# Kernel tuning notes

Measured on AMD Instinct MI355X. Metric: run time of the kernel, lower is better.

The kernel has to match this reference:

```python
import jax, jax.numpy as jnp
import numpy as np

L = 160        # voxel grid side
BATCH = 4
N_SAMPLE = 62500
N = 64


def _build_coords():
    rng = np.random.default_rng(0)
    coords = []
    for b in range(BATCH):
        c = np.unique(rng.integers(0, L, (N_SAMPLE, 3)), axis=0)  # sorted, unique
        bc = np.concatenate([np.full((len(c), 1), b, dtype=np.int64), c.astype(np.int64)], axis=1)
        coords.append(bc)
    return np.concatenate(coords, axis=0)  # [P,4] = (batch, x, y, z), globally key-sorted


def _neighbor_table(C):
    # integer key per coordinate; coords are unique+sorted so keys are strictly increasing
    keys = ((C[:, 0] * L + C[:, 1]) * L + C[:, 2]) * L + C[:, 3]
    P = C.shape[0]
    offs = np.array([[dx, dy, dz] for dx in (-1, 0, 1) for dy in (-1, 0, 1) for dz in (-1, 0, 1)], dtype=np.int64)
    nbr = np.full((P, 27), -1, dtype=np.int32)
    for k, o in enumerate(offs):
        nc = C[:, 1:] + o
        valid = np.all((nc >= 0) & (nc < L), axis=1)
        nk = ((C[:, 0] * L + nc[:, 0]) * L + nc[:, 1]) * L + nc[:, 2]
        pos = np.clip(np.searchsorted(keys, nk), 0, P - 1)
        found = valid & (keys[pos] == nk)
        nbr[:, k] = np.where(found, pos, -1).astype(np.int32)
    return nbr


def setup_inputs() -> dict:
    C = _build_coords()
    nbr = _neighbor_table(C)
    P = C.shape[0]
    key = jax.random.key(0)
    ks = jax.random.split(key, 10)
    s = 0.05  # small weight scale keeps activations well-conditioned
    return {
        "feats": jax.random.normal(ks[0], (P, N), jnp.float32),
        "cond": jax.random.normal(ks[1], (P, 2 * N), jnp.float32),
        "W1a": jax.random.normal(ks[2], (27, N, N), jnp.float32) * s,
        "b1a": jax.random.normal(ks[3], (N,), jnp.float32) * s,
        "W1b": jax.random.normal(ks[4], (27, N, N), jnp.float32) * s,
        "b1b": jax.random.normal(ks[5], (N,), jnp.float32) * s,
        "W2a": jax.random.normal(ks[6], (27, N, N), jnp.float32) * s,
        "b2a": jax.random.normal(ks[7], (N,), jnp.float32) * s,
        "W2b": jax.random.normal(ks[8], (27, N, N), jnp.float32) * s,
        "b2b": jax.random.normal(ks[9], (N,), jnp.float32) * s,
        "nbr": jnp.asarray(nbr),
    }


def _sparse_conv(x, nbr, W, b):
    # x: [P,N] features, nbr: [P,27] neighbor indices (-1 = missing)
    mask = (nbr >= 0)
    idx = jnp.maximum(nbr, 0)
    acc0 = jnp.zeros((x.shape[0], W.shape[2]), x.dtype)

    def body(acc, kin):
        wk, ik, mk = kin            # wk:[N,N], ik:[P], mk:[P]
        g = x[ik] * mk[:, None].astype(x.dtype)
        return acc + g @ wk, None

    out, _ = jax.lax.scan(body, acc0, (W, idx.T, mask.T))
    return out + b


def reference(feats, cond, W1a, b1a, W1b, b1b, W2a, b2a, W2b, b2b, nbr):
    x_res = feats
    # conv_1: conv -> relu -> conv
    h = _sparse_conv(feats, nbr, W1a, b1a)
    h = jax.nn.relu(h)
    h = _sparse_conv(h, nbr, W1b, b1b)
    # FiLM from condition (features_at_coordinates at identical coords -> direct lookup)
    beta, gamma = jnp.split(cond, 2, axis=1)
    h = h * beta + gamma
    # conv_2: conv -> relu -> conv -> relu
    h = _sparse_conv(h, nbr, W2a, b2a)
    h = jax.nn.relu(h)
    h = _sparse_conv(h, nbr, W2b, b2b)
    h = jax.nn.relu(h)
    # residual: x_res at same coordinates is an identity lookup
    return h + x_res
```

## Files before the change

### kernel.cpp

```cpp
#include <hip/hip_runtime.h>
#include <hip/hip_bf16.h>


#define N 64
#define TAPS 27
#define MT 256

typedef unsigned short u16;
typedef __attribute__((ext_vector_type(8))) short short8;
typedef __attribute__((ext_vector_type(16))) float floatx16;

__device__ __forceinline__ float bf2f(u16 v) {
    union { unsigned u; float f; } c;
    c.u = ((unsigned)v) << 16;
    return c.f;
}
__device__ __forceinline__ u16 f2bf(float f) {
    __hip_bfloat16 h = __float2bfloat16(f);
    u16 r;
    __builtin_memcpy(&r, &h, 2);
    return r;
}
__device__ __forceinline__ void split2(float x, u16& hi, u16& lo) {
    hi = f2bf(x);
    lo = f2bf(x - bf2f(hi));
}

__global__ void split_feats(const float* __restrict__ x, u16* __restrict__ hl, int n) {
    int i = blockIdx.x * 256 + threadIdx.x;
    if (i >= n) return;
    int p = i >> 6, c = i & 63;
    u16 h, l;
    split2(x[i], h, l);
    hl[(size_t)p * 128 + c] = h;
    hl[(size_t)p * 128 + 64 + c] = l;
}

__global__ void transpose_w(const float* __restrict__ W, u16* __restrict__ Wt) {
    const float* src = W + blockIdx.x * (N * N);
    u16* dst = Wt + blockIdx.x * (N * 128);
    int t = threadIdx.x;
#pragma unroll
    for (int m = 0; m < 16; ++m) {
        int e = t + m * 256;
        int i = e >> 6;
        int j = e & 63;
        u16 h, l;
        split2(src[e], h, l);
        dst[j * 128 + i] = h;
        dst[j * 128 + 64 + i] = l;
    }
}

template <int MODE>
__global__ __launch_bounds__(256, 2) void conv_k(
    const u16* __restrict__ Xhl, const u16* __restrict__ Wt,
    const float* __restrict__ bias, const int* __restrict__ nbr,
    const float* __restrict__ cond, const float* __restrict__ resid,
    u16* __restrict__ out_hl, float* __restrict__ out_f32, int P) {
    __shared__ __align__(16) u16 As[MT * 128];
    __shared__ __align__(16) u16 Bs[N * 128];

    const int tid = threadIdx.x;
    const int pbase = blockIdx.x * MT;

    const int tA = tid;
    const int prA = pbase + tA;
    const long nbrbase = (long)prA * TAPS;
    const int rB = tid >> 2;
    const int mB = tid & 3;

    const int w = tid >> 6;
    const int lane = tid & 63;
    const int cn = lane & 31;
    const int kh = lane >> 5;
    const int rowA0 = w * 64 + cn;

    floatx16 acc00, acc01, acc10, acc11;
#pragma unroll
    for (int i = 0; i < 16; ++i) { acc00[i] = 0.f; acc01[i] = 0.f; acc10[i] = 0.f; acc11[i] = 0.f; }

    int idx = (prA < P) ? nbr[nbrbase] : -1;

    const u16* wtap = Wt + (size_t)rB * 128;

    for (int k = 0; k < TAPS; ++k) {
        if (k) __syncthreads();

        {
            const bool valid = (idx >= 0);
            const u16* xrow = Xhl + (size_t)(valid ? idx : 0) * 128;
#pragma unroll
            for (int c = 0; c < 16; ++c) {
                const int s = (c + tA) & 15;
                const int src = (s >> 3) * 64 + (((s & 7) ^ (tA & 7)) * 8);
                uint4 v = make_uint4(0u, 0u, 0u, 0u);
                if (valid) v = *reinterpret_cast<const uint4*>(xrow + src);
                *reinterpret_cast<uint4*>(&As[tA * 128 + s * 8]) = v;
            }
        }
        {
            const u16* wrow = wtap + (size_t)k * (N * 128);
#pragma unroll
            for (int q = 0; q < 4; ++q) {
                const int s = (mB + 4 * q + rB) & 15;
                const int src = (s >> 3) * 64 + (((s & 7) ^ (rB & 7)) * 8);
                *reinterpret_cast<uint4*>(&Bs[rB * 128 + s * 8]) =
                    *reinterpret_cast<const uint4*>(wrow + src);
            }
        }
        idx = (k + 1 < TAPS && prA < P) ? nbr[nbrbase + k + 1] : -1;

        __syncthreads();

#pragma unroll
        for (int kc = 0; kc < 4; ++kc) {
            const int g = 2 * kc + kh;
            const int sw = (g ^ (cn & 7)) * 8;
            const short8 a_h0 = *reinterpret_cast<const short8*>(&As[rowA0 * 128 + sw]);
            const short8 a_l0 = *reinterpret_cast<const short8*>(&As[rowA0 * 128 + 64 + sw]);
            const short8 a_h1 = *reinterpret_cast<const short8*>(&As[(rowA0 + 32) * 128 + sw]);
            const short8 a_l1 = *reinterpret_cast<const short8*>(&As[(rowA0 + 32) * 128 + 64 + sw]);
            const short8 b_h0 = *reinterpret_cast<const short8*>(&Bs[cn * 128 + sw]);
            const short8 b_l0 = *reinterpret_cast<const short8*>(&Bs[cn * 128 + 64 + sw]);
            const short8 b_h1 = *reinterpret_cast<const short8*>(&Bs[(cn + 32) * 128 + sw]);
            const short8 b_l1 = *reinterpret_cast<const short8*>(&Bs[(cn + 32) * 128 + 64 + sw]);

            acc00 = __builtin_amdgcn_mfma_f32_32x32x16_bf16(a_h0, b_h0, acc00, 0, 0, 0);
            acc00 = __builtin_amdgcn_mfma_f32_32x32x16_bf16(a_h0, b_l0, acc00, 0, 0, 0);
            acc00 = __builtin_amdgcn_mfma_f32_32x32x16_bf16(a_l0, b_h0, acc00, 0, 0, 0);

            acc01 = __builtin_amdgcn_mfma_f32_32x32x16_bf16(a_h0, b_h1, acc01, 0, 0, 0);
            acc01 = __builtin_amdgcn_mfma_f32_32x32x16_bf16(a_h0, b_l1, acc01, 0, 0, 0);
            acc01 = __builtin_amdgcn_mfma_f32_32x32x16_bf16(a_l0, b_h1, acc01, 0, 0, 0);

            acc10 = __builtin_amdgcn_mfma_f32_32x32x16_bf16(a_h1, b_h0, acc10, 0, 0, 0);
            acc10 = __builtin_amdgcn_mfma_f32_32x32x16_bf16(a_h1, b_l0, acc10, 0, 0, 0);
            acc10 = __builtin_amdgcn_mfma_f32_32x32x16_bf16(a_l1, b_h0, acc10, 0, 0, 0);

            acc11 = __builtin_amdgcn_mfma_f32_32x32x16_bf16(a_h1, b_h1, acc11, 0, 0, 0);
            acc11 = __builtin_amdgcn_mfma_f32_32x32x16_bf16(a_h1, b_l1, acc11, 0, 0, 0);
            acc11 = __builtin_amdgcn_mfma_f32_32x32x16_bf16(a_l1, b_h1, acc11, 0, 0, 0);
        }
    }

    auto epi = [&](const floatx16& a, int mt, int nt) {
        const int j = nt * 32 + cn;
        const float bj = bias[j];
#pragma unroll
        for (int reg = 0; reg < 16; ++reg) {
            const int row = (reg & 3) + 8 * (reg >> 2) + 4 * kh;
            const int p = pbase + w * 64 + mt * 32 + row;
            if (p < P) {
                float o = a[reg] + bj;
                if (MODE == 0 || MODE == 2) o = fmaxf(o, 0.f);
                if (MODE == 1) {
                    const float be = cond[(size_t)p * (2 * N) + j];
                    const float ga = cond[(size_t)p * (2 * N) + N + j];
                    o = o * be + ga;
                }
                if (MODE == 3) {
                    o = fmaxf(o, 0.f) + resid[(size_t)p * N + j];
                    out_f32[(size_t)p * N + j] = o;
                } else {
                    u16 h, l;
                    split2(o, h, l);
                    out_hl[(size_t)p * 128 + j] = h;
                    out_hl[(size_t)p * 128 + 64 + j] = l;
                }
            }
        }
    };
    epi(acc00, 0, 0);
    epi(acc01, 0, 1);
    epi(acc10, 1, 0);
    epi(acc11, 1, 1);
}

extern "C" void kernel_launch(void* const* d_in, const int* in_sizes, int n_in,
                              void* d_out, int out_size, void* d_ws, size_t ws_size,
                              hipStream_t stream) {
    const float* feats = (const float*)d_in[0];
    const float* cond  = (const float*)d_in[1];
    const float* W1a   = (const float*)d_in[2];
    const float* b1a   = (const float*)d_in[3];
    const float* W1b   = (const float*)d_in[4];
    const float* b1b   = (const float*)d_in[5];
    const float* W2a   = (const float*)d_in[6];
    const float* b2a   = (const float*)d_in[7];
    const float* W2b   = (const float*)d_in[8];
    const float* b2b   = (const float*)d_in[9];
    const int* nbr     = (const int*)d_in[10];
    float* out = (float*)d_out;
    u16* out_hl = (u16*)d_out;

    const int P = in_sizes[0] / N;

    const size_t wtElems = (size_t)TAPS * N * 128;
    u16* wt0 = (u16*)d_ws;
    u16* wt1 = wt0 + wtElems;
    u16* wt2 = wt1 + wtElems;
    u16* wt3 = wt2 + wtElems;
    u16* hA  = wt3 + wtElems;

    transpose_w<<<TAPS, 256, 0, stream>>>(W1a, wt0);
    transpose_w<<<TAPS, 256, 0, stream>>>(W1b, wt1);
    transpose_w<<<TAPS, 256, 0, stream>>>(W2a, wt2);
    transpose_w<<<TAPS, 256, 0, stream>>>(W2b, wt3);
    split_feats<<<(P * N + 255) / 256, 256, 0, stream>>>(feats, out_hl, P * N);

    const int blocks = (P + MT - 1) / MT;
    conv_k<0><<<blocks, 256, 0, stream>>>(out_hl, wt0, b1a, nbr, nullptr, nullptr, hA, nullptr, P);
    conv_k<1><<<blocks, 256, 0, stream>>>(hA, wt1, b1b, nbr, cond, nullptr, out_hl, nullptr, P);
    conv_k<2><<<blocks, 256, 0, stream>>>(out_hl, wt2, b2a, nbr, nullptr, nullptr, hA, nullptr, P);
    conv_k<3><<<blocks, 256, 0, stream>>>(hA, wt3, b2b, nbr, nullptr, feats, nullptr, out, P);
}
```

Baseline: 1.262 ms.

## Gather neighbor rows directly into LDS with async global_load_lds

Replaces register-staged gathers of neighbor feature rows and weight tiles with direct global-to-LDS async loads. Each lane of a wave loads one 16-byte slot, and each row's source offset is swizzled so the LDS layout matches the existing bank-conflict-avoiding pattern. Weights are pre-swizzled on the host-side transpose kernel. Missing neighbors point at a zeroed scratch buffer. The aim is to cut VGPR round-trips and the instruction overhead of ds_write. The cost is 16 scalar nbr loads per lane per tap in place of one prefetched index per thread, and the next tap's index is no longer prefetched.

```diff
diff --git a/kernel.cpp b/kernel.cpp
--- a/kernel.cpp
+++ b/kernel.cpp
@@ -25,6 +25,14 @@
     hi = f2bf(x);
     lo = f2bf(x - bf2f(hi));
 }
+
+__device__ __forceinline__ void async16(u16* lds, const u16* g) {
+    __builtin_amdgcn_global_load_lds(
+        (const __attribute__((address_space(1))) unsigned int*)g,
+        (__attribute__((address_space(3))) unsigned int*)lds, 16, 0, 0);
+}
+
+__global__ void zero_zp(u16* zp) { zp[threadIdx.x] = 0; }
 
 __global__ void split_feats(const float* __restrict__ x, u16* __restrict__ hl, int n) {
     int i = blockIdx.x * 256 + threadIdx.x;
@@ -47,8 +55,9 @@
         int j = e & 63;
         u16 h, l;
         split2(src[e], h, l);
-        dst[j * 128 + i] = h;
-        dst[j * 128 + 64 + i] = l;
+        int x = (((i >> 3) ^ (j & 7)) * 8) + (i & 7);
+        dst[j * 128 + x] = h;
+        dst[j * 128 + 64 + x] = l;
     }
 }
 
@@ -57,18 +66,13 @@
     const u16* __restrict__ Xhl, const u16* __restrict__ Wt,
     const float* __restrict__ bias, const int* __restrict__ nbr,
     const float* __restrict__ cond, const float* __restrict__ resid,
+    const u16* __restrict__ zp,
     u16* __restrict__ out_hl, float* __restrict__ out_f32, int P) {
     __shared__ __align__(16) u16 As[MT * 128];
     __shared__ __align__(16) u16 Bs[N * 128];
 
     const int tid = threadIdx.x;
     const int pbase = blockIdx.x * MT;
-
-    const int tA = tid;
-    const int prA = pbase + tA;
-    const long nbrbase = (long)prA * TAPS;
-    const int rB = tid >> 2;
-    const int mB = tid & 3;
 
     const int w = tid >> 6;
     const int lane = tid & 63;
@@ -76,40 +80,40 @@
     const int kh = lane >> 5;
     const int rowA0 = w * 64 + cn;
 
+    const int lrow = lane >> 4;
+    const int lslot = lane & 15;
+    const int swzE = (lslot >> 3) * 64 + (((lslot & 7) ^ lrow) * 8);
+    const int swzO = (lslot >> 3) * 64 + (((lslot & 7) ^ (4 + lrow)) * 8);
+
     floatx16 acc00, acc01, acc10, acc11;
 #pragma unroll
     for (int i = 0; i < 16; ++i) { acc00[i] = 0.f; acc01[i] = 0.f; acc10[i] = 0.f; acc11[i] = 0.f; }
-
-    int idx = (prA < P) ? nbr[nbrbase] : -1;
-
-    const u16* wtap = Wt + (size_t)rB * 128;
 
     for (int k = 0; k < TAPS; ++k) {
         if (k) __syncthreads();
 
+        int ii[16];
+#pragma unroll
+        for (int i = 0; i < 16; ++i) {
+            const int pr = pbase + w * 64 + i * 4 + lrow;
+            const int pc = (pr < P) ? pr : (P - 1);
+            int v = nbr[(size_t)pc * TAPS + k];
+            ii[i] = (pr < P) ? v : -1;
+        }
+#pragma unroll
+        for (int i = 0; i < 16; ++i) {
+            const u16* s = (ii[i] >= 0)
+                ? Xhl + (size_t)ii[i] * 128 + ((i & 1) ? swzO : swzE)
+                : zp + lslot * 8;
+            async16(&As[(w * 64 + i * 4) * 128], s);
+        }
         {
-            const bool valid = (idx >= 0);
-            const u16* xrow = Xhl + (size_t)(valid ? idx : 0) * 128;
-#pragma unroll
-            for (int c = 0; c < 16; ++c) {
-                const int s = (c + tA) & 15;
-                const int src = (s >> 3) * 64 + (((s & 7) ^ (tA & 7)) * 8);
-                uint4 v = make_uint4(0u, 0u, 0u, 0u);
-                if (valid) v = *reinterpret_cast<const uint4*>(xrow + src);
-                *reinterpret_cast<uint4*>(&As[tA * 128 + s * 8]) = v;
+            const u16* wk = Wt + ((size_t)k * N + w * 16) * 128 + lane * 8;
+#pragma unroll
+            for (int q = 0; q < 4; ++q) {
+                async16(&Bs[(w * 16 + q * 4) * 128], wk + q * (4 * 128));
             }
         }
-        {
-            const u16* wrow = wtap + (size_t)k * (N * 128);
-#pragma unroll
-            for (int q = 0; q < 4; ++q) {
-                const int s = (mB + 4 * q + rB) & 15;
-                const int src = (s >> 3) * 64 + (((s & 7) ^ (rB & 7)) * 8);
-                *reinterpret_cast<uint4*>(&Bs[rB * 128 + s * 8]) =
-                    *reinterpret_cast<const uint4*>(wrow + src);
-            }
-        }
-        idx = (k + 1 < TAPS && prA < P) ? nbr[nbrbase + k + 1] : -1;
 
         __syncthreads();
 
@@ -197,12 +201,14 @@
     const int P = in_sizes[0] / N;
 
     const size_t wtElems = (size_t)TAPS * N * 128;
-    u16* wt0 = (u16*)d_ws;
+    u16* zp  = (u16*)d_ws;
+    u16* wt0 = zp + 128;
     u16* wt1 = wt0 + wtElems;
     u16* wt2 = wt1 + wtElems;
     u16* wt3 = wt2 + wtElems;
     u16* hA  = wt3 + wtElems;
 
+    zero_zp<<<1, 128, 0, stream>>>(zp);
     transpose_w<<<TAPS, 256, 0, stream>>>(W1a, wt0);
     transpose_w<<<TAPS, 256, 0, stream>>>(W1b, wt1);
     transpose_w<<<TAPS, 256, 0, stream>>>(W2a, wt2);
@@ -210,8 +216,8 @@
     split_feats<<<(P * N + 255) / 256, 256, 0, stream>>>(feats, out_hl, P * N);
 
     const int blocks = (P + MT - 1) / MT;
-    conv_k<0><<<blocks, 256, 0, stream>>>(out_hl, wt0, b1a, nbr, nullptr, nullptr, hA, nullptr, P);
-    conv_k<1><<<blocks, 256, 0, stream>>>(hA, wt1, b1b, nbr, cond, nullptr, out_hl, nullptr, P);
-    conv_k<2><<<blocks, 256, 0, stream>>>(out_hl, wt2, b2a, nbr, nullptr, nullptr, hA, nullptr, P);
-    conv_k<3><<<blocks, 256, 0, stream>>>(hA, wt3, b2b, nbr, nullptr, feats, nullptr, out, P);
-}
+    conv_k<0><<<blocks, 256, 0, stream>>>(out_hl, wt0, b1a, nbr, nullptr, nullptr, zp, hA, nullptr, P);
+    conv_k<1><<<blocks, 256, 0, stream>>>(hA, wt1, b1b, nbr, cond, nullptr, zp, out_hl, nullptr, P);
+    conv_k<2><<<blocks, 256, 0, stream>>>(out_hl, wt2, b2a, nbr, nullptr, nullptr, zp, hA, nullptr, P);
+    conv_k<3><<<blocks, 256, 0, stream>>>(hA, wt3, b2b, nbr, nullptr, feats, zp, nullptr, out, P);
+}
```

Result: faster. 1.116 ms (-11.5%).
